# Kernel tuning notes

Hardware: AMD Instinct MI355X
Metric: run time of the kernel (lower is better)

Reference implementation:

```python
import jax, jax.numpy as jnp
import numpy as np

N_RAYS = 131072          # rays in batch (e.g., 512x256 tile)
N_SAMPLES = 4194304      # total occupied samples after occ-grid culling (~32/ray)
STEP = 5e-3              # render_step_size (from render_step_size_vals)


def setup_inputs() -> dict:
    key = jax.random.key(0)
    k1, k2, k3, k4 = jax.random.split(key, 4)
    # sorted ray indices, as produced by occGrid.sampling (packed, ascending)
    ray_indices = jnp.sort(jax.random.randint(k1, (N_SAMPLES,), 0, N_RAYS)).astype(jnp.int32)
    t_starts = jax.random.uniform(k2, (N_SAMPLES,), jnp.float32) * 4.0
    t_ends = t_starts + STEP
    sigmas = jax.random.uniform(k3, (N_SAMPLES,), jnp.float32) * 50.0  # raw densities (density_scale=1)
    hdr = jax.random.uniform(k4, (N_SAMPLES, 3), jnp.float32)          # per-sample HDR radiance
    return {"t_starts": t_starts, "t_ends": t_ends, "sigmas": sigmas,
            "hdr": hdr, "ray_indices": ray_indices, "n_rays": N_RAYS}


def _render_and_accumulate(t_starts, t_ends, sigmas, hdr, ray_indices, n_rays):
    S = t_starts.shape[0]
    dt = t_ends - t_starts
    sdt = sigmas * dt                              # sigma * delta_t per sample
    alphas = 1.0 - jnp.exp(-sdt)                   # per-sample alpha
    # exclusive per-ray cumsum of sdt: global exclusive cumsum minus value at segment lead
    excl = jnp.cumsum(sdt) - sdt                   # global exclusive cumsum
    flag = jnp.concatenate([jnp.ones((1,), bool), ray_indices[1:] != ray_indices[:-1]])
    # index of the lead (first) sample of each ray segment, propagated forward
    lead = jax.lax.associative_scan(jnp.maximum, jnp.where(flag, jnp.arange(S), 0))
    trans = jnp.exp(-(excl - excl[lead]))          # transmittance T_i within each ray
    weights = trans * alphas                       # render_weight_from_density
    # accumulate_along_rays (segment reduce); indices are sorted
    opac = jax.ops.segment_sum(weights, ray_indices, num_segments=n_rays,
                               indices_are_sorted=True)                      # [n_rays]
    hdr_acc = jax.ops.segment_sum(weights[:, None] * hdr, ray_indices,
                                  num_segments=n_rays, indices_are_sorted=True)  # [n_rays,3]
    return jnp.concatenate([opac[:, None], hdr_acc], axis=-1)  # [n_rays, 4] = (opacity, hdr)


def reference(t_starts, t_ends, sigmas, hdr, ray_indices, n_rays):
    return _render_and_accumulate(t_starts, t_ends, sigmas, hdr, ray_indices, n_rays)
```

## Files before the change

### kernel.cpp

```cpp
#include <hip/hip_runtime.h>


#define TPB 256
#define LDSF (256 * 17)

#define DPP0(SRC, CTRL, RMASK, BC) __int_as_float(__builtin_amdgcn_update_dpp( \
        0, __float_as_int(SRC), (CTRL), (RMASK), 0xf, (BC)))

#define IMAXD(V, CTRL, RMASK, BC) { \
    int _tmp = __builtin_amdgcn_update_dpp(0, (V), (CTRL), (RMASK), 0xf, (BC)); \
    (V) = ((V) > _tmp) ? (V) : _tmp; }

__device__ __forceinline__ float fold16_dpp(float x) {
    float a = 0.0f;
    a = __fadd_rn(a, DPP0(x, 0x110 | 15, 0xf, true));
    a = __fadd_rn(a, DPP0(x, 0x110 | 14, 0xf, true));
    a = __fadd_rn(a, DPP0(x, 0x110 | 13, 0xf, true));
    a = __fadd_rn(a, DPP0(x, 0x110 | 12, 0xf, true));
    a = __fadd_rn(a, DPP0(x, 0x110 | 11, 0xf, true));
    a = __fadd_rn(a, DPP0(x, 0x110 | 10, 0xf, true));
    a = __fadd_rn(a, DPP0(x, 0x110 |  9, 0xf, true));
    a = __fadd_rn(a, DPP0(x, 0x110 |  8, 0xf, true));
    a = __fadd_rn(a, DPP0(x, 0x110 |  7, 0xf, true));
    a = __fadd_rn(a, DPP0(x, 0x110 |  6, 0xf, true));
    a = __fadd_rn(a, DPP0(x, 0x110 |  5, 0xf, true));
    a = __fadd_rn(a, DPP0(x, 0x110 |  4, 0xf, true));
    a = __fadd_rn(a, DPP0(x, 0x110 |  3, 0xf, true));
    a = __fadd_rn(a, DPP0(x, 0x110 |  2, 0xf, true));
    a = __fadd_rn(a, DPP0(x, 0x110 |  1, 0xf, true));
    a = __fadd_rn(a, x);
    return a;
}

__device__ __forceinline__ float wscan(float v) {
    v = __fadd_rn(v, DPP0(v, 0x111, 0xf, true));
    v = __fadd_rn(v, DPP0(v, 0x112, 0xf, true));
    v = __fadd_rn(v, DPP0(v, 0x114, 0xf, true));
    v = __fadd_rn(v, DPP0(v, 0x118, 0xf, true));
    v = __fadd_rn(v, DPP0(v, 0x142, 0xa, false));
    v = __fadd_rn(v, DPP0(v, 0x143, 0xc, false));
    return v;
}

__device__ __forceinline__ float sdt_c(float tsv, float tev, float sgv) {
    return __fmul_rn(sgv, __fsub_rn(tev, tsv));
}

__global__ void k_bottom(const float* __restrict__ ts, const float* __restrict__ te,
                         const float* __restrict__ sg, int S,
                         float* __restrict__ sdt, float* __restrict__ s1,
                         float* __restrict__ T1,
                         float4* __restrict__ out4, int n_rays) {
    __shared__ float lds[LDSF];
    int t = threadIdx.x;
    int tile = blockIdx.x;
    int gid = tile * TPB + t;
    if (gid < n_rays) out4[gid] = make_float4(0.f, 0.f, 0.f, 0.f);
    const float4* ts4 = (const float4*)ts;
    const float4* te4 = (const float4*)te;
    const float4* sg4 = (const float4*)sg;
    float4* sdt4 = (float4*)sdt;
    #pragma unroll
    for (int k = 0; k < 4; ++k) {
        int idx4 = tile * 1024 + k * 256 + t;
        float4 a = ts4[idx4], b = te4[idx4], c = sg4[idx4];
        float4 xo;
        xo.x = sdt_c(a.x, b.x, c.x);
        xo.y = sdt_c(a.y, b.y, c.y);
        xo.z = sdt_c(a.z, b.z, c.z);
        xo.w = sdt_c(a.w, b.w, c.w);
        sdt4[idx4] = xo;
        int fl = (k * 256 + t) << 2;
        int g0 = fl >> 4, j0 = fl & 15;
        float* p = &lds[g0 * 17 + j0];
        p[0] = xo.x; p[1] = xo.y; p[2] = xo.z; p[3] = xo.w;
    }
    __syncthreads();
    float acc = 0.0f;
    #pragma unroll
    for (int j = 0; j < 16; ++j) acc = __fadd_rn(acc, lds[t * 17 + j]);
    float acc2 = fold16_dpp(acc);
    int g = tile * 256 + t;
    s1[g] = acc2;
    if ((t & 15) == 15) T1[g >> 4] = acc2;
}

__global__ void k_mid(const float* __restrict__ T1, float* __restrict__ C2) {
    __shared__ float T2sh[1024];
    __shared__ float s3sh[1024];
    __shared__ float s4sh[64];
    __shared__ float T3sh[64];
    __shared__ float T4sh[4];
    __shared__ float C5sh[4];
    int t = threadIdx.x;
    const float4* T14 = (const float4*)T1;
    float s2l[16];
    float acc = 0.0f;
    #pragma unroll
    for (int k = 0; k < 4; ++k) {
        float4 v = T14[t * 4 + k];
        acc = __fadd_rn(acc, v.x); s2l[k * 4 + 0] = acc;
        acc = __fadd_rn(acc, v.y); s2l[k * 4 + 1] = acc;
        acc = __fadd_rn(acc, v.z); s2l[k * 4 + 2] = acc;
        acc = __fadd_rn(acc, v.w); s2l[k * 4 + 3] = acc;
    }
    T2sh[t] = acc;
    __syncthreads();
    if (t < 64) {
        float a3 = 0.0f;
        for (int j = 0; j < 16; ++j) { a3 = __fadd_rn(a3, T2sh[t * 16 + j]); s3sh[t * 16 + j] = a3; }
        T3sh[t] = a3;
    }
    __syncthreads();
    if (t < 4) {
        float a4 = 0.0f;
        for (int j = 0; j < 16; ++j) { a4 = __fadd_rn(a4, T3sh[t * 16 + j]); s4sh[t * 16 + j] = a4; }
        T4sh[t] = a4;
    }
    __syncthreads();
    if (t == 0) {
        float c = 0.0f;
        for (int r = 0; r < 4; ++r) { c = __fadd_rn(c, T4sh[r]); C5sh[r] = c; }
    }
    __syncthreads();
    if (t < 64) {
        int r = t >> 4;
        float v4 = s4sh[t];
        s4sh[t] = r ? __fadd_rn(v4, C5sh[r - 1]) : v4;
    }
    __syncthreads();
    {
        int r = t >> 4;
        float v3 = s3sh[t];
        float c3 = r ? __fadd_rn(v3, s4sh[r - 1]) : v3;
        s3sh[t] = c3;
    }
    __syncthreads();
    float c3m = t ? s3sh[t - 1] : 0.0f;
    float4* C24 = (float4*)C2;
    #pragma unroll
    for (int k = 0; k < 4; ++k) {
        float4 o;
        o.x = t ? __fadd_rn(s2l[k * 4 + 0], c3m) : s2l[k * 4 + 0];
        o.y = t ? __fadd_rn(s2l[k * 4 + 1], c3m) : s2l[k * 4 + 1];
        o.z = t ? __fadd_rn(s2l[k * 4 + 2], c3m) : s2l[k * 4 + 2];
        o.w = t ? __fadd_rn(s2l[k * 4 + 3], c3m) : s2l[k * 4 + 3];
        C24[t * 4 + k] = o;
    }
}

__global__ void k_render(const int* __restrict__ ri, const float* __restrict__ sdt,
                         const float* __restrict__ s1, const float* __restrict__ C2,
                         const float* __restrict__ hdr,
                         int S, float* __restrict__ out) {
    const int tid = blockIdx.x * TPB + threadIdx.x;
    const int t = threadIdx.x & 63;
    const int i0 = tid * 4;
    const bool valid = i0 < S;

    float4 xq = valid ? ((const float4*)sdt)[tid] : make_float4(0.f, 0.f, 0.f, 0.f);
    int4 rq;
    if (valid) rq = ((const int4*)ri)[tid];
    else { rq.x = rq.y = rq.z = rq.w = -1 - t; }

    int dpr = __builtin_amdgcn_update_dpp(0, rq.w, 0x111, 0xf, 0xf, true);
    int prev_r = dpr;
    if ((t & 15) == 0) prev_r = (i0 == 0 || !valid) ? (rq.x ^ 1) : ri[i0 - 1];

    bool f0 = prev_r != rq.x;
    bool f1 = rq.y != rq.x;
    bool f2 = rq.z != rq.y;
    bool f3 = rq.w != rq.z;
    unsigned long long mask0 = __ballot(f0);

    int q = t & 3;
    float p0 = __fadd_rn(0.0f, xq.x);
    float p1 = __fadd_rn(p0, xq.y);
    float p2 = __fadd_rn(p1, xq.z);
    float p3 = __fadd_rn(p2, xq.w);
    float pf = p3;
    #pragma unroll
    for (int rr = 1; rr <= 3; ++rr) {
        float cin = DPP0(pf, 0x111, 0xf, true);
        float n0 = __fadd_rn(cin, xq.x);
        float n1 = __fadd_rn(n0, xq.y);
        float n2 = __fadd_rn(n1, xq.z);
        float n3 = __fadd_rn(n2, xq.w);
        bool me = (q == rr);
        p0 = me ? n0 : p0;
        p1 = me ? n1 : p1;
        p2 = me ? n2 : p2;
        p3 = me ? n3 : p3;
        pf = me ? n3 : pf;
    }

    int g = i0 >> 4;
    float cj = 0.0f;
    if (valid && g) {
        int j3 = g - 1;
        cj = (j3 >> 4) ? __fadd_rn(s1[j3], C2[(j3 >> 4) - 1]) : s1[j3];
    }
    float C0 = g ? __fadd_rn(p0, cj) : p0;
    float C1v = g ? __fadd_rn(p1, cj) : p1;
    float C2v = g ? __fadd_rn(p2, cj) : p2;
    float C3v = g ? __fadd_rn(p3, cj) : p3;
    float e0 = __fsub_rn(C0, xq.x);
    float e1 = __fsub_rn(C1v, xq.y);
    float e2 = __fsub_rn(C2v, xq.z);
    float e3 = __fsub_rn(C3v, xq.w);

    float el_lead = 0.0f;
    if (!(mask0 & 1ull)) {
        int wbs = (tid - t) * 4;
        int r0v = __builtin_amdgcn_readfirstlane(rq.x);
        int h0 = 0;
        for (int round = 0; round < 65536; ++round) {
            int idx = wbs - 1 - t - 64 * round;
            int rv = (idx >= 0) ? ri[idx] : (r0v ^ 1);
            unsigned long long mm = __ballot(rv != r0v);
            if (mm) {
                int lm = __ffsll((unsigned long long)mm) - 1;
                h0 = wbs - 64 * round - lm;
                break;
            }
        }
        float elv = 0.0f;
        if (t == 0) {
            const float4* s4 = (const float4*)sdt;
            int gh = h0 >> 4, lh = h0 & 15;
            float4 q0 = s4[gh * 4 + 0], q1 = s4[gh * 4 + 1];
            float4 q2 = s4[gh * 4 + 2], q3 = s4[gh * 4 + 3];
            float vv[16] = { q0.x, q0.y, q0.z, q0.w, q1.x, q1.y, q1.z, q1.w,
                             q2.x, q2.y, q2.z, q2.w, q3.x, q3.y, q3.z, q3.w };
            float a2 = 0.0f, xl = 0.0f;
            #pragma unroll
            for (int j2 = 0; j2 < 16; ++j2) {
                if (j2 <= lh) { a2 = __fadd_rn(a2, vv[j2]); xl = vv[j2]; }
            }
            float Ch = a2;
            if (gh) {
                int j3b = gh - 1;
                float cjb = (j3b >> 4) ? __fadd_rn(s1[j3b], C2[(j3b >> 4) - 1]) : s1[j3b];
                Ch = __fadd_rn(a2, cjb);
            }
            elv = __fsub_rn(Ch, xl);
        }
        el_lead = __int_as_float(__builtin_amdgcn_readfirstlane(__float_as_int(elv)));
    }

    int lh0 = f0 ? 0 : -1;
    int lh1 = f1 ? 1 : lh0;
    int lh2 = f2 ? 2 : lh1;
    int lh3 = f3 ? 3 : lh2;

    int key = (lh3 >= 0) ? (t + 1) : 0;
    int sk = __shfl_up(key, 1, 64);
    if (t == 0) sk = 0;
    int M = sk;
    IMAXD(M, 0x111, 0xf, true)
    IMAXD(M, 0x112, 0xf, true)
    IMAXD(M, 0x114, 0xf, true)
    IMAXD(M, 0x118, 0xf, true)
    IMAXD(M, 0x142, 0xa, false)
    IMAXD(M, 0x143, 0xc, false)
    int src = M;
    int psrc = (src > 0) ? (src - 1) : t;

    float el_last = (lh3 == 3) ? e3 : (lh3 == 2) ? e2 : (lh3 == 1) ? e1 : e0;
    float rel = __shfl(el_last, psrc, 64);
    float el_prev = (src > 0) ? rel : el_lead;

    float el0 = (lh0 >= 0) ? e0 : el_prev;
    float el1 = (lh1 == 1) ? e1 : ((lh1 == 0) ? e0 : el_prev);
    float el2 = (lh2 == 2) ? e2 : ((lh2 == 1) ? e1 : ((lh2 == 0) ? e0 : el_prev));
    float el3 = (lh3 == 3) ? e3 : ((lh3 == 2) ? e2 : ((lh3 == 1) ? e1 :
                ((lh3 == 0) ? e0 : el_prev)));

    float4 h0v, h1v, h2v;
    if (valid) {
        const float4* h4 = (const float4*)hdr;
        h0v = h4[3 * tid + 0]; h1v = h4[3 * tid + 1]; h2v = h4[3 * tid + 2];
    } else {
        h0v = h1v = h2v = make_float4(0.f, 0.f, 0.f, 0.f);
    }
    float w0 = 0.f, w1 = 0.f, w2 = 0.f, w3 = 0.f;
    if (valid) {
        w0 = __fmul_rn(__expf(-__fsub_rn(e0, el0)), __fsub_rn(1.0f, __expf(-xq.x)));
        w1 = __fmul_rn(__expf(-__fsub_rn(e1, el1)), __fsub_rn(1.0f, __expf(-xq.y)));
        w2 = __fmul_rn(__expf(-__fsub_rn(e2, el2)), __fsub_rn(1.0f, __expf(-xq.z)));
        w3 = __fmul_rn(__expf(-__fsub_rn(e3, el3)), __fsub_rn(1.0f, __expf(-xq.w)));
    }
    float4 v0 = make_float4(w0, __fmul_rn(w0, h0v.x), __fmul_rn(w0, h0v.y), __fmul_rn(w0, h0v.z));
    float4 v1 = make_float4(w1, __fmul_rn(w1, h0v.w), __fmul_rn(w1, h1v.x), __fmul_rn(w1, h1v.y));
    float4 v2 = make_float4(w2, __fmul_rn(w2, h1v.z), __fmul_rn(w2, h1v.w), __fmul_rn(w2, h2v.x));
    float4 v3 = make_float4(w3, __fmul_rn(w3, h2v.y), __fmul_rn(w3, h2v.z), __fmul_rn(w3, h2v.w));

    float4 V0 = v0;
    float4 V1 = make_float4(V0.x + v1.x, V0.y + v1.y, V0.z + v1.z, V0.w + v1.w);
    float4 V2 = make_float4(V1.x + v2.x, V1.y + v2.y, V1.z + v2.z, V1.w + v2.w);
    float4 V3 = make_float4(V2.x + v3.x, V2.y + v3.y, V2.z + v3.z, V2.w + v3.w);

    float4 W;
    W.x = wscan(V3.x); W.y = wscan(V3.y); W.z = wscan(V3.z); W.w = wscan(V3.w);
    float4 E;
    E.x = __shfl_up(W.x, 1, 64);
    E.y = __shfl_up(W.y, 1, 64);
    E.z = __shfl_up(W.z, 1, 64);
    E.w = __shfl_up(W.w, 1, 64);
    if (t == 0) { E.x = 0.f; E.y = 0.f; E.z = 0.f; E.w = 0.f; }

    float4 Vm1 = (lh3 == 1) ? V0 : ((lh3 == 2) ? V1 : V2);
    float4 bs_last;
    if (lh3 > 0) {
        bs_last = make_float4(E.x + Vm1.x, E.y + Vm1.y, E.z + Vm1.z, E.w + Vm1.w);
    } else {
        bs_last = E;
    }
    float4 rbs;
    rbs.x = __shfl(bs_last.x, psrc, 64);
    rbs.y = __shfl(bs_last.y, psrc, 64);
    rbs.z = __shfl(bs_last.z, psrc, 64);
    rbs.w = __shfl(bs_last.w, psrc, 64);
    float4 bs_prev = (src > 0) ? rbs : make_float4(0.f, 0.f, 0.f, 0.f);

    bool t0 = f1, t1 = f2, t2 = f3;
    bool t3 = (t < 63) ? (((mask0 >> (t + 1)) & 1ull) != 0ull) : true;

    if (valid) {
        #pragma unroll
        for (int j = 0; j < 4; ++j) {
            bool tl = (j == 0) ? t0 : (j == 1) ? t1 : (j == 2) ? t2 : t3;
            if (!tl) continue;
            int lhj = (j == 0) ? lh0 : (j == 1) ? lh1 : (j == 2) ? lh2 : lh3;
            float4 Vj = (j == 0) ? V0 : (j == 1) ? V1 : (j == 2) ? V2 : V3;
            int rj = (j == 0) ? rq.x : (j == 1) ? rq.y : (j == 2) ? rq.z : rq.w;
            float4 bsj;
            if (lhj >= 0) {
                if (lhj > 0) {
                    float4 Vh = (lhj == 1) ? V0 : ((lhj == 2) ? V1 : V2);
                    bsj = make_float4(E.x + Vh.x, E.y + Vh.y, E.z + Vh.z, E.w + Vh.w);
                } else {
                    bsj = E;
                }
            } else {
                bsj = bs_prev;
            }
            float px = (E.x + Vj.x) - bsj.x;
            float py = (E.y + Vj.y) - bsj.y;
            float pz = (E.z + Vj.z) - bsj.z;
            float pw = (E.w + Vj.w) - bsj.w;
            if (rj >= 0) {
                float* o = out + 4 * rj;
                atomicAdd(o + 0, px);
                atomicAdd(o + 1, py);
                atomicAdd(o + 2, pz);
                atomicAdd(o + 3, pw);
            }
        }
    }
}

extern "C" void kernel_launch(void* const* d_in, const int* in_sizes, int n_in,
                              void* d_out, int out_size, void* d_ws, size_t ws_size,
                              hipStream_t stream) {
    const float* ts  = (const float*)d_in[0];
    const float* te  = (const float*)d_in[1];
    const float* sg  = (const float*)d_in[2];
    const float* hdr = (const float*)d_in[3];
    const int*   ri  = (const int*)d_in[4];
    const int S      = in_sizes[0];
    const int n_rays = out_size / 4;
    const int N1 = S >> 4;
    const int N2 = N1 >> 4;

    char* w = (char*)d_ws;
    auto alloc = [&](size_t bytes) { char* p = w; w += (bytes + 255) & ~255ULL; return p; };
    float* sdt = (float*)alloc((size_t)S * 4);
    float* s1  = (float*)alloc((size_t)N1 * 4);
    float* T1  = (float*)alloc((size_t)N2 * 4);
    float* C2  = (float*)alloc((size_t)N2 * 4);

    k_bottom<<<dim3(N1 / TPB), dim3(TPB), 0, stream>>>(ts, te, sg, S, sdt, s1, T1,
                                                       (float4*)d_out, n_rays);
    k_mid   <<<dim3(1), dim3(1024), 0, stream>>>(T1, C2);
    k_render<<<dim3(S / (TPB * 4)), dim3(TPB), 0, stream>>>(ri, sdt, s1, C2, hdr, S, (float*)d_out);
}
```

Measured before the change: 164.9 us.

## Process eight samples per thread in render kernel with simplified segment logic

The render kernel now handles eight samples per thread instead of four, loading two float4s of sdt and ray indices and six float4s of hdr per thread. The intra-16-sample scan drops from a four-round DPP carry chain to a single DPP step between lane pairs. Lead and segment-base selection is rewritten as chained selects over per-sample flags instead of the lh index comparisons. The grid shrinks by half, which amortizes wave-level scans and shuffles over more samples, at the cost of higher register pressure and fewer waves for latency hiding.

New measurement: 167.7 us. No clear change (+1.7%).

```diff
diff --git a/kernel.cpp b/kernel.cpp
--- a/kernel.cpp
+++ b/kernel.cpp
@@ -10,6 +10,8 @@
 #define IMAXD(V, CTRL, RMASK, BC) { \
     int _tmp = __builtin_amdgcn_update_dpp(0, (V), (CTRL), (RMASK), 0xf, (BC)); \
     (V) = ((V) > _tmp) ? (V) : _tmp; }
+
+#define ADD4(A, B) make_float4((A).x + (B).x, (A).y + (B).y, (A).z + (B).z, (A).w + (B).w)
 
 __device__ __forceinline__ float fold16_dpp(float x) {
     float a = 0.0f;
@@ -155,43 +157,53 @@
                          int S, float* __restrict__ out) {
     const int tid = blockIdx.x * TPB + threadIdx.x;
     const int t = threadIdx.x & 63;
-    const int i0 = tid * 4;
+    const int i0 = tid * 8;
     const bool valid = i0 < S;
 
-    float4 xq = valid ? ((const float4*)sdt)[tid] : make_float4(0.f, 0.f, 0.f, 0.f);
-    int4 rq;
-    if (valid) rq = ((const int4*)ri)[tid];
-    else { rq.x = rq.y = rq.z = rq.w = -1 - t; }
-
-    int dpr = __builtin_amdgcn_update_dpp(0, rq.w, 0x111, 0xf, 0xf, true);
+    float4 xa, xb; int4 ra, rb;
+    if (valid) {
+        xa = ((const float4*)sdt)[2 * tid];
+        xb = ((const float4*)sdt)[2 * tid + 1];
+        ra = ((const int4*)ri)[2 * tid];
+        rb = ((const int4*)ri)[2 * tid + 1];
+    } else {
+        xa = xb = make_float4(0.f, 0.f, 0.f, 0.f);
+        ra.x = ra.y = ra.z = ra.w = -1 - t;
+        rb = ra;
+    }
+
+    int dpr = __builtin_amdgcn_update_dpp(0, rb.w, 0x111, 0xf, 0xf, true);
     int prev_r = dpr;
-    if ((t & 15) == 0) prev_r = (i0 == 0 || !valid) ? (rq.x ^ 1) : ri[i0 - 1];
-
-    bool f0 = prev_r != rq.x;
-    bool f1 = rq.y != rq.x;
-    bool f2 = rq.z != rq.y;
-    bool f3 = rq.w != rq.z;
+    if ((t & 15) == 0) prev_r = (i0 == 0 || !valid) ? (ra.x ^ 1) : ri[i0 - 1];
+
+    bool f0 = prev_r != ra.x;
+    bool f1 = ra.y != ra.x, f2 = ra.z != ra.y, f3 = ra.w != ra.z;
+    bool f4 = rb.x != ra.w, f5 = rb.y != rb.x, f6 = rb.z != rb.y, f7 = rb.w != rb.z;
     unsigned long long mask0 = __ballot(f0);
 
-    int q = t & 3;
-    float p0 = __fadd_rn(0.0f, xq.x);
-    float p1 = __fadd_rn(p0, xq.y);
-    float p2 = __fadd_rn(p1, xq.z);
-    float p3 = __fadd_rn(p2, xq.w);
-    float pf = p3;
-    #pragma unroll
-    for (int rr = 1; rr <= 3; ++rr) {
-        float cin = DPP0(pf, 0x111, 0xf, true);
-        float n0 = __fadd_rn(cin, xq.x);
-        float n1 = __fadd_rn(n0, xq.y);
-        float n2 = __fadd_rn(n1, xq.z);
-        float n3 = __fadd_rn(n2, xq.w);
-        bool me = (q == rr);
-        p0 = me ? n0 : p0;
-        p1 = me ? n1 : p1;
-        p2 = me ? n2 : p2;
-        p3 = me ? n3 : p3;
-        pf = me ? n3 : pf;
+    float p0 = __fadd_rn(0.0f, xa.x);
+    float p1 = __fadd_rn(p0, xa.y);
+    float p2 = __fadd_rn(p1, xa.z);
+    float p3 = __fadd_rn(p2, xa.w);
+    float p4 = __fadd_rn(p3, xb.x);
+    float p5 = __fadd_rn(p4, xb.y);
+    float p6 = __fadd_rn(p5, xb.z);
+    float p7 = __fadd_rn(p6, xb.w);
+    {
+        float cin = DPP0(p7, 0x111, 0xf, true);
+        float n0 = __fadd_rn(cin, xa.x);
+        float n1 = __fadd_rn(n0, xa.y);
+        float n2 = __fadd_rn(n1, xa.z);
+        float n3 = __fadd_rn(n2, xa.w);
+        float n4 = __fadd_rn(n3, xb.x);
+        float n5 = __fadd_rn(n4, xb.y);
+        float n6 = __fadd_rn(n5, xb.z);
+        float n7 = __fadd_rn(n6, xb.w);
+        bool me = (t & 1) != 0;
+        p0 = me ? n0 : p0; p1 = me ? n1 : p1;
+        p2 = me ? n2 : p2; p3 = me ? n3 : p3;
+        p4 = me ? n4 : p4; p5 = me ? n5 : p5;
+        p6 = me ? n6 : p6; p7 = me ? n7 : p7;
     }
 
     int g = i0 >> 4;
@@ -200,19 +212,19 @@
         int j3 = g - 1;
         cj = (j3 >> 4) ? __fadd_rn(s1[j3], C2[(j3 >> 4) - 1]) : s1[j3];
     }
-    float C0 = g ? __fadd_rn(p0, cj) : p0;
-    float C1v = g ? __fadd_rn(p1, cj) : p1;
-    float C2v = g ? __fadd_rn(p2, cj) : p2;
-    float C3v = g ? __fadd_rn(p3, cj) : p3;
-    float e0 = __fsub_rn(C0, xq.x);
-    float e1 = __fsub_rn(C1v, xq.y);
-    float e2 = __fsub_rn(C2v, xq.z);
-    float e3 = __fsub_rn(C3v, xq.w);
+    float e0 = __fsub_rn(g ? __fadd_rn(p0, cj) : p0, xa.x);
+    float e1 = __fsub_rn(g ? __fadd_rn(p1, cj) : p1, xa.y);
+    float e2 = __fsub_rn(g ? __fadd_rn(p2, cj) : p2, xa.z);
+    float e3 = __fsub_rn(g ? __fadd_rn(p3, cj) : p3, xa.w);
+    float e4 = __fsub_rn(g ? __fadd_rn(p4, cj) : p4, xb.x);
+    float e5 = __fsub_rn(g ? __fadd_rn(p5, cj) : p5, xb.y);
+    float e6 = __fsub_rn(g ? __fadd_rn(p6, cj) : p6, xb.z);
+    float e7 = __fsub_rn(g ? __fadd_rn(p7, cj) : p7, xb.w);
 
     float el_lead = 0.0f;
     if (!(mask0 & 1ull)) {
-        int wbs = (tid - t) * 4;
-        int r0v = __builtin_amdgcn_readfirstlane(rq.x);
+        int wbs = (tid - t) * 8;
+        int r0v = __builtin_amdgcn_readfirstlane(ra.x);
         int h0 = 0;
         for (int round = 0; round < 65536; ++round) {
             int idx = wbs - 1 - t - 64 * round;
@@ -248,12 +260,10 @@
         el_lead = __int_as_float(__builtin_amdgcn_readfirstlane(__float_as_int(elv)));
     }
 
-    int lh0 = f0 ? 0 : -1;
-    int lh1 = f1 ? 1 : lh0;
-    int lh2 = f2 ? 2 : lh1;
-    int lh3 = f3 ? 3 : lh2;
-
-    int key = (lh3 >= 0) ? (t + 1) : 0;
+    bool hb0 = f0, hb1 = f1 | hb0, hb2 = f2 | hb1, hb3 = f3 | hb2;
+    bool hb4 = f4 | hb3, hb5 = f5 | hb4, hb6 = f6 | hb5, hb7 = f7 | hb6;
+
+    int key = (valid && hb7) ? (t + 1) : 0;
     int sk = __shfl_up(key, 1, 64);
     if (t == 0) sk = 0;
     int M = sk;
@@ -266,42 +276,60 @@
     int src = M;
     int psrc = (src > 0) ? (src - 1) : t;
 
-    float el_last = (lh3 == 3) ? e3 : (lh3 == 2) ? e2 : (lh3 == 1) ? e1 : e0;
-    float rel = __shfl(el_last, psrc, 64);
+    float el7c = f7 ? e7 : f6 ? e6 : f5 ? e5 : f4 ? e4 :
+                 f3 ? e3 : f2 ? e2 : f1 ? e1 : f0 ? e0 : 0.0f;
+    float rel = __shfl(el7c, psrc, 64);
     float el_prev = (src > 0) ? rel : el_lead;
 
-    float el0 = (lh0 >= 0) ? e0 : el_prev;
-    float el1 = (lh1 == 1) ? e1 : ((lh1 == 0) ? e0 : el_prev);
-    float el2 = (lh2 == 2) ? e2 : ((lh2 == 1) ? e1 : ((lh2 == 0) ? e0 : el_prev));
-    float el3 = (lh3 == 3) ? e3 : ((lh3 == 2) ? e2 : ((lh3 == 1) ? e1 :
-                ((lh3 == 0) ? e0 : el_prev)));
-
-    float4 h0v, h1v, h2v;
+    float el0 = f0 ? e0 : el_prev;
+    float el1 = f1 ? e1 : el0;
+    float el2 = f2 ? e2 : el1;
+    float el3 = f3 ? e3 : el2;
+    float el4 = f4 ? e4 : el3;
+    float el5 = f5 ? e5 : el4;
+    float el6 = f6 ? e6 : el5;
+    float el7 = f7 ? e7 : el6;
+
+    float4 h0v, h1v, h2v, h3v, h4v, h5v;
     if (valid) {
         const float4* h4 = (const float4*)hdr;
-        h0v = h4[3 * tid + 0]; h1v = h4[3 * tid + 1]; h2v = h4[3 * tid + 2];
+        h0v = h4[6 * tid + 0]; h1v = h4[6 * tid + 1]; h2v = h4[6 * tid + 2];
+        h3v = h4[6 * tid + 3]; h4v = h4[6 * tid + 4]; h5v = h4[6 * tid + 5];
     } else {
-        h0v = h1v = h2v = make_float4(0.f, 0.f, 0.f, 0.f);
+        h0v = h1v = h2v = h3v = h4v = h5v = make_float4(0.f, 0.f, 0.f, 0.f);
     }
     float w0 = 0.f, w1 = 0.f, w2 = 0.f, w3 = 0.f;
+    float w4 = 0.f, w5 = 0.f, w6 = 0.f, w7 = 0.f;
     if (valid) {
-        w0 = __fmul_rn(__expf(-__fsub_rn(e0, el0)), __fsub_rn(1.0f, __expf(-xq.x)));
-        w1 = __fmul_rn(__expf(-__fsub_rn(e1, el1)), __fsub_rn(1.0f, __expf(-xq.y)));
-        w2 = __fmul_rn(__expf(-__fsub_rn(e2, el2)), __fsub_rn(1.0f, __expf(-xq.z)));
-        w3 = __fmul_rn(__expf(-__fsub_rn(e3, el3)), __fsub_rn(1.0f, __expf(-xq.w)));
+        w0 = __fmul_rn(__expf(-__fsub_rn(e0, el0)), __fsub_rn(1.0f, __expf(-xa.x)));
+        w1 = __fmul_rn(__expf(-__fsub_rn(e1, el1)), __fsub_rn(1.0f, __expf(-xa.y)));
+        w2 = __fmul_rn(__expf(-__fsub_rn(e2, el2)), __fsub_rn(1.0f, __expf(-xa.z)));
+        w3 = __fmul_rn(__expf(-__fsub_rn(e3, el3)), __fsub_rn(1.0f, __expf(-xa.w)));
+        w4 = __fmul_rn(__expf(-__fsub_rn(e4, el4)), __fsub_rn(1.0f, __expf(-xb.x)));
+        w5 = __fmul_rn(__expf(-__fsub_rn(e5, el5)), __fsub_rn(1.0f, __expf(-xb.y)));
+        w6 = __fmul_rn(__expf(-__fsub_rn(e6, el6)), __fsub_rn(1.0f, __expf(-xb.z)));
+        w7 = __fmul_rn(__expf(-__fsub_rn(e7, el7)), __fsub_rn(1.0f, __expf(-xb.w)));
     }
     float4 v0 = make_float4(w0, __fmul_rn(w0, h0v.x), __fmul_rn(w0, h0v.y), __fmul_rn(w0, h0v.z));
     float4 v1 = make_float4(w1, __fmul_rn(w1, h0v.w), __fmul_rn(w1, h1v.x), __fmul_rn(w1, h1v.y));
     float4 v2 = make_float4(w2, __fmul_rn(w2, h1v.z), __fmul_rn(w2, h1v.w), __fmul_rn(w2, h2v.x));
     float4 v3 = make_float4(w3, __fmul_rn(w3, h2v.y), __fmul_rn(w3, h2v.z), __fmul_rn(w3, h2v.w));
+    float4 v4 = make_float4(w4, __fmul_rn(w4, h3v.x), __fmul_rn(w4, h3v.y), __fmul_rn(w4, h3v.z));
+    float4 v5 = make_float4(w5, __fmul_rn(w5, h3v.w), __fmul_rn(w5, h4v.x), __fmul_rn(w5, h4v.y));
+    float4 v6 = make_float4(w6, __fmul_rn(w6, h4v.z), __fmul_rn(w6, h4v.w), __fmul_rn(w6, h5v.x));
+    float4 v7 = make_float4(w7, __fmul_rn(w7, h5v.y), __fmul_rn(w7, h5v.z), __fmul_rn(w7, h5v.w));
 
     float4 V0 = v0;
-    float4 V1 = make_float4(V0.x + v1.x, V0.y + v1.y, V0.z + v1.z, V0.w + v1.w);
-    float4 V2 = make_float4(V1.x + v2.x, V1.y + v2.y, V1.z + v2.z, V1.w + v2.w);
-    float4 V3 = make_float4(V2.x + v3.x, V2.y + v3.y, V2.z + v3.z, V2.w + v3.w);
+    float4 V1 = ADD4(V0, v1);
+    float4 V2 = ADD4(V1, v2);
+    float4 V3 = ADD4(V2, v3);
+    float4 V4 = ADD4(V3, v4);
+    float4 V5 = ADD4(V4, v5);
+    float4 V6 = ADD4(V5, v6);
+    float4 V7 = ADD4(V6, v7);
 
     float4 W;
-    W.x = wscan(V3.x); W.y = wscan(V3.y); W.z = wscan(V3.z); W.w = wscan(V3.w);
+    W.x = wscan(V7.x); W.y = wscan(V7.y); W.z = wscan(V7.z); W.w = wscan(V7.w);
     float4 E;
     E.x = __shfl_up(W.x, 1, 64);
     E.y = __shfl_up(W.y, 1, 64);
@@ -309,55 +337,44 @@
     E.w = __shfl_up(W.w, 1, 64);
     if (t == 0) { E.x = 0.f; E.y = 0.f; E.z = 0.f; E.w = 0.f; }
 
-    float4 Vm1 = (lh3 == 1) ? V0 : ((lh3 == 2) ? V1 : V2);
-    float4 bs_last;
-    if (lh3 > 0) {
-        bs_last = make_float4(E.x + Vm1.x, E.y + Vm1.y, E.z + Vm1.z, E.w + Vm1.w);
-    } else {
-        bs_last = E;
-    }
+    float4 Z = make_float4(0.f, 0.f, 0.f, 0.f);
+    float4 B0 = f0 ? E : Z;
+    float4 B1 = f1 ? ADD4(E, V0) : B0;
+    float4 B2 = f2 ? ADD4(E, V1) : B1;
+    float4 B3 = f3 ? ADD4(E, V2) : B2;
+    float4 B4 = f4 ? ADD4(E, V3) : B3;
+    float4 B5 = f5 ? ADD4(E, V4) : B4;
+    float4 B6 = f6 ? ADD4(E, V5) : B5;
+    float4 B7 = f7 ? ADD4(E, V6) : B6;
+
     float4 rbs;
-    rbs.x = __shfl(bs_last.x, psrc, 64);
-    rbs.y = __shfl(bs_last.y, psrc, 64);
-    rbs.z = __shfl(bs_last.z, psrc, 64);
-    rbs.w = __shfl(bs_last.w, psrc, 64);
-    float4 bs_prev = (src > 0) ? rbs : make_float4(0.f, 0.f, 0.f, 0.f);
-
-    bool t0 = f1, t1 = f2, t2 = f3;
-    bool t3 = (t < 63) ? (((mask0 >> (t + 1)) & 1ull) != 0ull) : true;
-
-    if (valid) {
-        #pragma unroll
-        for (int j = 0; j < 4; ++j) {
-            bool tl = (j == 0) ? t0 : (j == 1) ? t1 : (j == 2) ? t2 : t3;
-            if (!tl) continue;
-            int lhj = (j == 0) ? lh0 : (j == 1) ? lh1 : (j == 2) ? lh2 : lh3;
-            float4 Vj = (j == 0) ? V0 : (j == 1) ? V1 : (j == 2) ? V2 : V3;
-            int rj = (j == 0) ? rq.x : (j == 1) ? rq.y : (j == 2) ? rq.z : rq.w;
-            float4 bsj;
-            if (lhj >= 0) {
-                if (lhj > 0) {
-                    float4 Vh = (lhj == 1) ? V0 : ((lhj == 2) ? V1 : V2);
-                    bsj = make_float4(E.x + Vh.x, E.y + Vh.y, E.z + Vh.z, E.w + Vh.w);
-                } else {
-                    bsj = E;
-                }
-            } else {
-                bsj = bs_prev;
-            }
-            float px = (E.x + Vj.x) - bsj.x;
-            float py = (E.y + Vj.y) - bsj.y;
-            float pz = (E.z + Vj.z) - bsj.z;
-            float pw = (E.w + Vj.w) - bsj.w;
-            if (rj >= 0) {
-                float* o = out + 4 * rj;
-                atomicAdd(o + 0, px);
-                atomicAdd(o + 1, py);
-                atomicAdd(o + 2, pz);
-                atomicAdd(o + 3, pw);
-            }
-        }
-    }
+    rbs.x = __shfl(B7.x, psrc, 64);
+    rbs.y = __shfl(B7.y, psrc, 64);
+    rbs.z = __shfl(B7.z, psrc, 64);
+    rbs.w = __shfl(B7.w, psrc, 64);
+    float4 bs_prev = (src > 0) ? rbs : Z;
+
+    bool tl0 = f1, tl1 = f2, tl2 = f3, tl3 = f4, tl4 = f5, tl5 = f6, tl6 = f7;
+    bool tl7 = (t < 63) ? (((mask0 >> (t + 1)) & 1ull) != 0ull) : true;
+
+#define EMIT(K, TLK, RJ, VK) \
+    if (valid && (TLK) && (RJ) >= 0) { \
+        float4 bse = hb##K ? B##K : bs_prev; \
+        float* o = out + 4 * (RJ); \
+        atomicAdd(o + 0, (E.x + (VK).x) - bse.x); \
+        atomicAdd(o + 1, (E.y + (VK).y) - bse.y); \
+        atomicAdd(o + 2, (E.z + (VK).z) - bse.z); \
+        atomicAdd(o + 3, (E.w + (VK).w) - bse.w); \
+    }
+    EMIT(0, tl0, ra.x, V0)
+    EMIT(1, tl1, ra.y, V1)
+    EMIT(2, tl2, ra.z, V2)
+    EMIT(3, tl3, ra.w, V3)
+    EMIT(4, tl4, rb.x, V4)
+    EMIT(5, tl5, rb.y, V5)
+    EMIT(6, tl6, rb.z, V6)
+    EMIT(7, tl7, rb.w, V7)
+#undef EMIT
 }
 
 extern "C" void kernel_launch(void* const* d_in, const int* in_sizes, int n_in,
@@ -383,5 +400,5 @@
     k_bottom<<<dim3(N1 / TPB), dim3(TPB), 0, stream>>>(ts, te, sg, S, sdt, s1, T1,
                                                        (float4*)d_out, n_rays);
     k_mid   <<<dim3(1), dim3(1024), 0, stream>>>(T1, C2);
-    k_render<<<dim3(S / (TPB * 4)), dim3(TPB), 0, stream>>>(ri, sdt, s1, C2, hdr, S, (float*)d_out);
-}
+    k_render<<<dim3(S / (TPB * 8)), dim3(TPB), 0, stream>>>(ri, sdt, s1, C2, hdr, S, (float*)d_out);
+}
```
